# Performance work log

Measured on AMD Instinct MI355X. Metric: run time of the kernel, lower is better.

The kernel has to match this reference:

```python
import jax, jax.numpy as jnp
import numpy as np

HEAD, D_MODEL, D_KV = 16, 1024, 64
B, NQ, NK = 2, 2048, 2048


def setup_inputs() -> dict:
    key = jax.random.key(0)
    ks = jax.random.split(key, 10)
    s = 1.0 / np.sqrt(D_MODEL)
    return {
        "queries": jax.random.normal(ks[0], (B, NQ, D_MODEL), jnp.float32),
        "keys": jax.random.normal(ks[1], (B, NK, D_MODEL), jnp.float32),
        "values": jax.random.normal(ks[2], (B, NK, D_MODEL), jnp.float32),
        "group_prob": jax.random.uniform(ks[3], (B, 1, NQ, NK), jnp.float32),
        "attention_mask": jnp.ones((B, NK), jnp.int32),
        "Wq": jax.random.normal(ks[4], (D_MODEL, HEAD * D_KV), jnp.float32) * s,
        "bq": jnp.zeros((HEAD * D_KV,), jnp.float32),
        "Wk": jax.random.normal(ks[5], (D_MODEL, HEAD * D_KV), jnp.float32) * s,
        "bk": jnp.zeros((HEAD * D_KV,), jnp.float32),
        "Wv": jax.random.normal(ks[6], (D_MODEL, HEAD * D_KV), jnp.float32) * s,
        "bv": jnp.zeros((HEAD * D_KV,), jnp.float32),
    }


def reference(queries, keys, values, group_prob, attention_mask, Wq, bq, Wk, bk, Wv, bv):
    b_s, nq, _ = queries.shape
    nk = keys.shape[1]
    # projections -> [b, h, n, d]
    q = (queries @ Wq + bq).reshape(b_s, nq, HEAD, D_KV).transpose(0, 2, 1, 3)
    k = (keys @ Wk + bk).reshape(b_s, nk, HEAD, D_KV).transpose(0, 2, 1, 3)
    v = (values @ Wv + bv).reshape(b_s, nk, HEAD, D_KV).transpose(0, 2, 1, 3)
    att = jnp.einsum("bhqd,bhkd->bhqk", q, k) / np.sqrt(D_KV).astype(np.float32)
    # NOTE: original uses non-in-place `att.masked_fill(...)` and discards the
    # result, so attention_mask has NO effect on the computation. Replicated.
    att = jax.nn.softmax(att, axis=-1)
    att = att * group_prob  # post-softmax group gating, broadcast over heads
    out = jnp.einsum("bhqk,bhkd->bhqd", att, v)
    return out.transpose(0, 2, 1, 3).reshape(b_s, nq, D_MODEL)
```

## Files before the change

kernel.cpp:

```cpp
#include <hip/hip_runtime.h>
#include <hip/hip_bf16.h>
#include <cstdint>

typedef unsigned short ushort_t;
typedef __attribute__((ext_vector_type(8))) short short8;
typedef __attribute__((ext_vector_type(4))) float floatx4;
typedef __attribute__((ext_vector_type(4))) unsigned short ushort4_t;

#define H_   16
#define DKV_ 64
#define DM_  1024
#define B_   2
#define NQ_  2048
#define NK_  2048

__device__ __forceinline__ unsigned short f2bf(float f) {
  union { float f; unsigned int u; } v; v.f = f;
  unsigned int u = v.u;
  return (unsigned short)((u + 0x7fffu + ((u >> 16) & 1u)) >> 16);
}

__device__ __forceinline__ float fexp2(float x) { return __builtin_amdgcn_exp2f(x); }
__device__ __forceinline__ float frcp(float x)  { return __builtin_amdgcn_rcpf(x); }

__device__ __forceinline__ floatx4 mfma16(short8 a, short8 b, floatx4 c) {
  return __builtin_amdgcn_mfma_f32_16x16x32_bf16(a, b, c, 0, 0, 0);
}

__device__ __forceinline__ void gload_lds16(const ushort_t* g, ushort_t* l) {
  __builtin_amdgcn_global_load_lds(
      (const __attribute__((address_space(1))) void*)g,
      (__attribute__((address_space(3))) void*)l, 16, 0, 0);
}

__global__ __launch_bounds__(256) void cast_x_kernel(
    const float* __restrict__ q, const float* __restrict__ k,
    const float* __restrict__ v, ushort_t* __restrict__ dst)
{
  const int t = blockIdx.y;
  const float* src = (t == 0) ? q : (t == 1) ? k : v;
  ushort_t* d = dst + (size_t)t * 4096 * 1024;
  const int gid = blockIdx.x * 256 + threadIdx.x;
  #pragma unroll
  for (int u = 0; u < 8; u++) {
    const int i4 = u * 131072 + gid;
    floatx4 f = ((const floatx4*)src)[i4];
    ushort4_t o;
    #pragma unroll
    for (int e = 0; e < 4; e++) o[e] = f2bf(f[e]);
    *(ushort4_t*)&d[(size_t)i4 * 4] = o;
  }
}

__global__ __launch_bounds__(256) void cast_wt_kernel(
    const float* __restrict__ Wq, const float* __restrict__ Wk,
    const float* __restrict__ Wv, ushort_t* __restrict__ WtAll)
{
  __shared__ ushort_t tile[32][33];
  const int t = blockIdx.z;
  const float* W = (t == 0) ? Wq : (t == 1) ? Wk : Wv;
  ushort_t* Wt = WtAll + (size_t)t * 1024 * 1024;
  const int n0 = blockIdx.x * 32, k0 = blockIdx.y * 32;
  const int tid = threadIdx.x, r = tid >> 3, c4 = (tid & 7) * 4;
  floatx4 f = *(const floatx4*)&W[(size_t)(k0 + r) * 1024 + n0 + c4];
  #pragma unroll
  for (int e = 0; e < 4; e++) tile[r][c4 + e] = f2bf(f[e]);
  __syncthreads();
  ushort4_t o;
  #pragma unroll
  for (int e = 0; e < 4; e++) o[e] = tile[c4 + e][r];
  *(ushort4_t*)&Wt[(size_t)(n0 + r) * 1024 + k0 + c4] = o;
}

__global__ __launch_bounds__(256, 2) void proj_kernel2(
    const ushort_t* __restrict__ Xbf, const ushort_t* __restrict__ WtAll,
    const float* __restrict__ bq, const float* __restrict__ bk,
    const float* __restrict__ bv,
    ushort_t* __restrict__ Qb, ushort_t* __restrict__ Kb, ushort_t* __restrict__ Vt)
{
  const int mode = blockIdx.z;
  const ushort_t* X  = Xbf  + (size_t)mode * 4096 * 1024;
  const ushort_t* Wt = WtAll + (size_t)mode * 1024 * 1024;
  const float* bias  = (mode == 0) ? bq : (mode == 1) ? bk : bv;
  ushort_t* dst      = (mode == 0) ? Qb : (mode == 1) ? Kb : Vt;

  __shared__ ushort_t SM[8192];
  ushort_t* SA = SM;
  ushort_t* SB = SM + 4096;

  const int tid = threadIdx.x, lane = tid & 63, wid = tid >> 6;
  const int c = lane & 15, g = lane >> 4;
  const int m0 = blockIdx.y * 128, n0 = blockIdx.x * 128;
  const int wm = wid & 1, wn = wid >> 1, mb = wm * 64, nb = wn * 64;
  const int srow = lane >> 2;
  const int schunk = (lane & 3) * 8;

  floatx4 acc[4][4];
  #pragma unroll
  for (int i = 0; i < 4; i++)
    #pragma unroll
    for (int j = 0; j < 4; j++) acc[i][j] = floatx4{0.f, 0.f, 0.f, 0.f};

  for (int k0 = 0; k0 < DM_; k0 += 32) {
    __syncthreads();
    #pragma unroll
    for (int u = 0; u < 2; u++) {
      const int t = wid * 2 + u;
      gload_lds16(&X [(size_t)(m0 + t * 16 + srow) * 1024 + k0 + schunk], &SA[t * 512]);
      gload_lds16(&Wt[(size_t)(n0 + t * 16 + srow) * 1024 + k0 + schunk], &SB[t * 512]);
    }
    __syncthreads();

    short8 af[4], bfr[4];
    #pragma unroll
    for (int i = 0; i < 4; i++) af[i]  = *(const short8*)&SA[(mb + i * 16 + c) * 32 + g * 8];
    #pragma unroll
    for (int j = 0; j < 4; j++) bfr[j] = *(const short8*)&SB[(nb + j * 16 + c) * 32 + g * 8];
    #pragma unroll
    for (int i = 0; i < 4; i++)
      #pragma unroll
      for (int j = 0; j < 4; j++) acc[i][j] = mfma16(af[i], bfr[j], acc[i][j]);
  }

  __syncthreads();
  const float scale = (mode == 0) ? 0.18033688011112042f : 1.0f;
  ushort_t* EP = SM + wid * 2048;
  const int hh = (n0 + nb) >> 6;

  if (mode != 2) {
    for (int jj = 0; jj < 2; jj++) {
      #pragma unroll
      for (int jt = 0; jt < 2; jt++) {
        const int j = jj * 2 + jt;
        const float bb = bias[n0 + nb + j * 16 + c];
        #pragma unroll
        for (int i = 0; i < 4; i++)
          #pragma unroll
          for (int r = 0; r < 4; r++)
            EP[(i * 16 + g * 4 + r) * 32 + jt * 16 + c] =
                f2bf((acc[i][j][r] + bb) * scale);
      }
      #pragma unroll
      for (int u = 0; u < 8; u++) {
        const int rowl = u * 8 + (lane >> 3);
        ushort4_t vv = *(ushort4_t*)&EP[rowl * 32 + (lane & 7) * 4];
        const int rowg = m0 + mb + rowl;
        const int bb2 = rowg >> 11, nn = rowg & 2047;
        *(ushort4_t*)&dst[((size_t)(bb2 * H_ + hh) * NQ_ + nn) * DKV_ +
                          jj * 32 + (lane & 7) * 4] = vv;
      }
    }
  } else {
    const int bb2 = (m0 + mb) >> 11, nloc = (m0 + mb) & 2047;
    for (int j = 0; j < 4; j++) {
      const float bb = bias[n0 + nb + j * 16 + c];
      #pragma unroll
      for (int i = 0; i < 4; i++) {
        ushort4_t pk;
        #pragma unroll
        for (int r = 0; r < 4; r++) pk[r] = f2bf(acc[i][j][r] + bb);
        *(ushort4_t*)&EP[c * 72 + i * 16 + g * 4] = pk;
      }
      const int d0 = j * 16;
      #pragma unroll
      for (int u = 0; u < 2; u++) {
        const int coll = u * 8 + (lane >> 3);
        short8 vv = *(const short8*)&EP[coll * 72 + (lane & 7) * 8];
        *(short8*)&dst[((size_t)(bb2 * H_ + hh) * DKV_ + d0 + coll) * NK_ +
                       nloc + (lane & 7) * 8] = vv;
      }
    }
  }
}

constexpr int LDT = 40;
__global__ __launch_bounds__(256, 2) void proj_kernel_fb(
    const float* __restrict__ Xq, const float* __restrict__ Xk, const float* __restrict__ Xv,
    const float* __restrict__ Wq, const float* __restrict__ Wk, const float* __restrict__ Wv,
    const float* __restrict__ bq, const float* __restrict__ bk, const float* __restrict__ bv,
    ushort_t* __restrict__ Qb, ushort_t* __restrict__ Kb, ushort_t* __restrict__ Vt)
{
  const int mode = blockIdx.z;
  const float* X    = (mode == 0) ? Xq : (mode == 1) ? Xk : Xv;
  const float* W    = (mode == 0) ? Wq : (mode == 1) ? Wk : Wv;
  const float* bias = (mode == 0) ? bq : (mode == 1) ? bk : bv;
  ushort_t* dst     = (mode == 0) ? Qb : (mode == 1) ? Kb : Vt;

  __shared__ ushort_t Asm[128 * LDT];
  __shared__ ushort_t Bsm[128 * LDT];

  const int tid = threadIdx.x, lane = tid & 63, wid = tid >> 6;
  const int m0 = blockIdx.y * 128, n0 = blockIdx.x * 128;
  const int c = lane & 15, g = lane >> 4;
  const int wm = wid & 1, wn = wid >> 1, mb = wm * 64, nb = wn * 64;

  floatx4 acc[4][4];
  #pragma unroll
  for (int i = 0; i < 4; i++)
    #pragma unroll
    for (int j = 0; j < 4; j++) acc[i][j] = floatx4{0.f, 0.f, 0.f, 0.f};

  const int ar = tid >> 1, ah = tid & 1;
  const int bn = tid & 127, bh2 = tid >> 7;

  for (int k0 = 0; k0 < DM_; k0 += 32) {
    const floatx4* ap = (const floatx4*)(X + (size_t)(m0 + ar) * DM_ + k0 + ah * 16);
    floatx4 av0 = ap[0], av1 = ap[1], av2 = ap[2], av3 = ap[3];
    const float* wp = W + (size_t)(k0 + bh2 * 16) * 1024 + n0 + bn;
    float wv[16];
    #pragma unroll
    for (int j = 0; j < 16; j++) wv[j] = wp[j * 1024];
    short8 pa0, pa1, pb0, pb1;
    #pragma unroll
    for (int j = 0; j < 4; j++) {
      pa0[j] = (short)f2bf(av0[j]); pa0[4 + j] = (short)f2bf(av1[j]);
      pa1[j] = (short)f2bf(av2[j]); pa1[4 + j] = (short)f2bf(av3[j]);
    }
    #pragma unroll
    for (int j = 0; j < 8; j++) { pb0[j] = (short)f2bf(wv[j]); pb1[j] = (short)f2bf(wv[8 + j]); }
    __syncthreads();
    *(short8*)&Asm[ar * LDT + ah * 16]      = pa0;
    *(short8*)&Asm[ar * LDT + ah * 16 + 8]  = pa1;
    *(short8*)&Bsm[bn * LDT + bh2 * 16]     = pb0;
    *(short8*)&Bsm[bn * LDT + bh2 * 16 + 8] = pb1;
    __syncthreads();
    short8 af[4], bfr[4];
    #pragma unroll
    for (int i = 0; i < 4; i++) af[i]  = *(const short8*)&Asm[(mb + i * 16 + c) * LDT + g * 8];
    #pragma unroll
    for (int j = 0; j < 4; j++) bfr[j] = *(const short8*)&Bsm[(nb + j * 16 + c) * LDT + g * 8];
    #pragma unroll
    for (int i = 0; i < 4; i++)
      #pragma unroll
      for (int j = 0; j < 4; j++) acc[i][j] = mfma16(af[i], bfr[j], acc[i][j]);
  }
  #pragma unroll
  for (int j = 0; j < 4; j++) {
    const int col = n0 + nb + j * 16 + c;
    const float bv_ = bias[col];
    const int h = col >> 6, d = col & 63;
    #pragma unroll
    for (int i = 0; i < 4; i++)
      #pragma unroll
      for (int r = 0; r < 4; r++) {
        const int row = m0 + mb + i * 16 + g * 4 + r;
        const int b = row >> 11, n = row & 2047;
        float v = acc[i][j][r] + bv_;
        if (mode == 0) {
          v *= 0.18033688011112042f;
          dst[((size_t)(b * H_ + h) * NQ_ + n) * DKV_ + d] = f2bf(v);
        } else if (mode == 1) {
          dst[((size_t)(b * H_ + h) * NQ_ + n) * DKV_ + d] = f2bf(v);
        } else {
          dst[((size_t)(b * H_ + h) * DKV_ + d) * NK_ + n] = f2bf(v);
        }
      }
  }
}

__global__ __launch_bounds__(256, 2) void attn_kernel(
    const ushort_t* __restrict__ Qb, const ushort_t* __restrict__ Kb,
    const ushort_t* __restrict__ Vt, const float* __restrict__ gp,
    float* __restrict__ out)
{
  __shared__ ushort_t Ks[2][64 * 72];
  __shared__ ushort_t Vs[2][64 * 72];
  __shared__ ushort_t Pl[4][32 * 72];

  const int tid = threadIdx.x, lane = tid & 63, wid = tid >> 6;
  const int c = lane & 15, g = lane >> 4;
  const int h = blockIdx.x, b = blockIdx.z;
  const int bh = b * H_ + h;
  const int qw = blockIdx.y * 128 + wid * 32;

  const ushort_t* Qp = Qb + (size_t)bh * NQ_ * DKV_;
  const ushort_t* Kp = Kb + (size_t)bh * NK_ * DKV_;
  const ushort_t* Vp = Vt + (size_t)bh * DKV_ * NK_;
  const float* gpp = gp + (size_t)b * NQ_ * NK_ + (size_t)qw * NK_;
  ushort_t* Pw = Pl[wid];

  const int srow = wid * 16 + (lane >> 2);
  const int scol = (lane & 3) * 8;

  short8 qf[2][2];
  #pragma unroll
  for (int i = 0; i < 2; i++)
    #pragma unroll
    for (int kc = 0; kc < 2; kc++)
      qf[i][kc] = *(const short8*)&Qp[(qw + i * 16 + c) * DKV_ + kc * 32 + g * 8];

  #pragma unroll
  for (int half = 0; half < 2; half++) {
    short8 kv = *(const short8*)&Kp[(size_t)srow * DKV_ + scol + half * 32];
    short8 vv = *(const short8*)&Vp[(size_t)srow * NK_ + scol + half * 32];
    *(short8*)&Ks[0][srow * 72 + scol + half * 32] = kv;
    *(short8*)&Vs[0][srow * 72 + scol + half * 32] = vv;
  }
  __syncthreads();

  floatx4 o[2][4];
  float l[2][4];
  #pragma unroll
  for (int i = 0; i < 2; i++) {
    #pragma unroll
    for (int jd = 0; jd < 4; jd++) o[i][jd] = floatx4{0.f, 0.f, 0.f, 0.f};
    #pragma unroll
    for (int r = 0; r < 4; r++) l[i][r] = 0.f;
  }

  for (int t = 0; t < NK_ / 64; t++) {
    const int k0 = t * 64;
    const int cur = t & 1, nxt = cur ^ 1;

    float gpv[2][4][4];
    #pragma unroll
    for (int i = 0; i < 2; i++)
      #pragma unroll
      for (int r = 0; r < 4; r++) {
        const float* gq = gpp + (size_t)(i * 16 + g * 4 + r) * NK_ + k0 + c;
        #pragma unroll
        for (int jk = 0; jk < 4; jk++) gpv[i][jk][r] = gq[jk * 16];
      }

    short8 knx[2], vnx[2];
    const bool has_next = (t + 1) < NK_ / 64;
    if (has_next) {
      const int k1 = k0 + 64;
      #pragma unroll
      for (int half = 0; half < 2; half++) {
        knx[half] = *(const short8*)&Kp[(size_t)(k1 + srow) * DKV_ + scol + half * 32];
        vnx[half] = *(const short8*)&Vp[(size_t)srow * NK_ + k1 + scol + half * 32];
      }
    }

    floatx4 s[2][4];
    #pragma unroll
    for (int i = 0; i < 2; i++)
      #pragma unroll
      for (int jk = 0; jk < 4; jk++) s[i][jk] = floatx4{0.f, 0.f, 0.f, 0.f};
    #pragma unroll
    for (int jk = 0; jk < 4; jk++) {
      #pragma unroll
      for (int kc = 0; kc < 2; kc++) {
        short8 kf = *(const short8*)&Ks[cur][(jk * 16 + c) * 72 + kc * 32 + g * 8];
        #pragma unroll
        for (int i = 0; i < 2; i++) s[i][jk] = mfma16(qf[i][kc], kf, s[i][jk]);
      }
    }

    #pragma unroll
    for (int i = 0; i < 2; i++)
      #pragma unroll
      for (int jk = 0; jk < 4; jk++)
        #pragma unroll
        for (int r = 0; r < 4; r++) {
          const float p = fexp2(s[i][jk][r]);
          l[i][r] += p;
          Pw[(i * 16 + g * 4 + r) * 72 + jk * 16 + c] = f2bf(p * gpv[i][jk][r]);
        }

    #pragma unroll
    for (int kc = 0; kc < 2; kc++) {
      short8 af0 = *(const short8*)&Pw[(0 * 16 + c) * 72 + kc * 32 + g * 8];
      short8 af1 = *(const short8*)&Pw[(1 * 16 + c) * 72 + kc * 32 + g * 8];
      #pragma unroll
      for (int jd = 0; jd < 4; jd++) {
        short8 vf = *(const short8*)&Vs[cur][(jd * 16 + c) * 72 + kc * 32 + g * 8];
        o[0][jd] = mfma16(af0, vf, o[0][jd]);
        o[1][jd] = mfma16(af1, vf, o[1][jd]);
      }
    }

    if (has_next) {
      #pragma unroll
      for (int half = 0; half < 2; half++) {
        *(short8*)&Ks[nxt][srow * 72 + scol + half * 32] = knx[half];
        *(short8*)&Vs[nxt][srow * 72 + scol + half * 32] = vnx[half];
      }
    }
    __syncthreads();
  }

  float invl[2][4];
  #pragma unroll
  for (int i = 0; i < 2; i++)
    #pragma unroll
    for (int r = 0; r < 4; r++) {
      float rs = l[i][r];
      rs += __shfl_xor(rs, 1);
      rs += __shfl_xor(rs, 2);
      rs += __shfl_xor(rs, 4);
      rs += __shfl_xor(rs, 8);
      invl[i][r] = frcp(rs);
    }
  #pragma unroll
  for (int i = 0; i < 2; i++)
    #pragma unroll
    for (int jd = 0; jd < 4; jd++)
      #pragma unroll
      for (int r = 0; r < 4; r++) {
        const int row = qw + i * 16 + g * 4 + r;
        out[(size_t)(b * NQ_ + row) * 1024 + h * 64 + jd * 16 + c] =
            o[i][jd][r] * invl[i][r];
      }
}

extern "C" void kernel_launch(void* const* d_in, const int* in_sizes, int n_in,
                              void* d_out, int out_size, void* d_ws, size_t ws_size,
                              hipStream_t stream) {
  const float* queries = (const float*)d_in[0];
  const float* keys    = (const float*)d_in[1];
  const float* values  = (const float*)d_in[2];
  const float* gp      = (const float*)d_in[3];
  const float* Wq = (const float*)d_in[5];
  const float* bq = (const float*)d_in[6];
  const float* Wk = (const float*)d_in[7];
  const float* bk = (const float*)d_in[8];
  const float* Wv = (const float*)d_in[9];
  const float* bv = (const float*)d_in[10];

  const size_t SZ_QKV = (size_t)3 * B_ * H_ * NQ_ * DKV_;
  const size_t SZ_X   = (size_t)3 * 4096 * 1024;
  const size_t SZ_W   = (size_t)3 * 1024 * 1024;
  const size_t NEED   = (SZ_QKV + SZ_X + SZ_W) * sizeof(ushort_t);

  ushort_t* Qb = (ushort_t*)d_ws;
  ushort_t* Kb = Qb + (size_t)B_ * H_ * NQ_ * DKV_;
  ushort_t* Vt = Kb + (size_t)B_ * H_ * NK_ * DKV_;
  float* out = (float*)d_out;

  if (ws_size >= NEED) {
    ushort_t* Xbf = Qb + SZ_QKV;
    ushort_t* Wt  = Xbf + SZ_X;
    cast_x_kernel<<<dim3(512, 3), 256, 0, stream>>>(queries, keys, values, Xbf);
    cast_wt_kernel<<<dim3(32, 32, 3), 256, 0, stream>>>(Wq, Wk, Wv, Wt);
    proj_kernel2<<<dim3(8, 32, 3), 256, 0, stream>>>(
        Xbf, Wt, bq, bk, bv, Qb, Kb, Vt);
  } else {
    proj_kernel_fb<<<dim3(8, 32, 3), 256, 0, stream>>>(
        queries, keys, values, Wq, Wk, Wv, bq, bk, bv, Qb, Kb, Vt);
  }
  attn_kernel<<<dim3(H_, NQ_ / 128, B_), 256, 0, stream>>>(Qb, Kb, Vt, gp, out);
}
```

Baseline: 252.9 us.

## Split attention block into 8 waves of 16 query rows with swizzled P tile

The attention kernel now runs 512 threads per block, with each of 8 waves owning 16 query rows instead of 4 waves owning 32. K/V tile staging is spread across all 512 threads, one short8 per thread. The per-wave P scratch is smaller and uses an XOR column swizzle on write and read to cut LDS bank conflicts. This lowers registers per wave and raises the number of waves available to hide latency, but each K/V fragment read from LDS now feeds half as many MFMAs, so LDS traffic per FLOP goes up.

```diff
diff --git a/kernel.cpp b/kernel.cpp
--- a/kernel.cpp
+++ b/kernel.cpp
@@ -258,20 +258,20 @@
   }
 }
 
-__global__ __launch_bounds__(256, 2) void attn_kernel(
+__global__ __launch_bounds__(512, 4) void attn_kernel(
     const ushort_t* __restrict__ Qb, const ushort_t* __restrict__ Kb,
     const ushort_t* __restrict__ Vt, const float* __restrict__ gp,
     float* __restrict__ out)
 {
   __shared__ ushort_t Ks[2][64 * 72];
   __shared__ ushort_t Vs[2][64 * 72];
-  __shared__ ushort_t Pl[4][32 * 72];
+  __shared__ ushort_t Pl[8][16 * 72];
 
   const int tid = threadIdx.x, lane = tid & 63, wid = tid >> 6;
   const int c = lane & 15, g = lane >> 4;
   const int h = blockIdx.x, b = blockIdx.z;
   const int bh = b * H_ + h;
-  const int qw = blockIdx.y * 128 + wid * 32;
+  const int qw = blockIdx.y * 128 + wid * 16;
 
   const ushort_t* Qp = Qb + (size_t)bh * NQ_ * DKV_;
   const ushort_t* Kp = Kb + (size_t)bh * NK_ * DKV_;
@@ -279,130 +279,105 @@
   const float* gpp = gp + (size_t)b * NQ_ * NK_ + (size_t)qw * NK_;
   ushort_t* Pw = Pl[wid];
 
-  const int srow = wid * 16 + (lane >> 2);
-  const int scol = (lane & 3) * 8;
-
-  short8 qf[2][2];
-  #pragma unroll
-  for (int i = 0; i < 2; i++)
-    #pragma unroll
-    for (int kc = 0; kc < 2; kc++)
-      qf[i][kc] = *(const short8*)&Qp[(qw + i * 16 + c) * DKV_ + kc * 32 + g * 8];
-
-  #pragma unroll
-  for (int half = 0; half < 2; half++) {
-    short8 kv = *(const short8*)&Kp[(size_t)srow * DKV_ + scol + half * 32];
-    short8 vv = *(const short8*)&Vp[(size_t)srow * NK_ + scol + half * 32];
-    *(short8*)&Ks[0][srow * 72 + scol + half * 32] = kv;
-    *(short8*)&Vs[0][srow * 72 + scol + half * 32] = vv;
-  }
+  const int gx16 = (g >> 1) << 4;
+  const int prd  = g ^ (((c >> 3) & 1) << 1);
+
+  const int srow = tid >> 3;
+  const int scol = (tid & 7) * 8;
+
+  short8 qf[2];
+  #pragma unroll
+  for (int kc = 0; kc < 2; kc++)
+    qf[kc] = *(const short8*)&Qp[(qw + c) * DKV_ + kc * 32 + g * 8];
+
+  *(short8*)&Ks[0][srow * 72 + scol] = *(const short8*)&Kp[(size_t)srow * DKV_ + scol];
+  *(short8*)&Vs[0][srow * 72 + scol] = *(const short8*)&Vp[(size_t)srow * NK_ + scol];
   __syncthreads();
 
-  floatx4 o[2][4];
-  float l[2][4];
-  #pragma unroll
-  for (int i = 0; i < 2; i++) {
-    #pragma unroll
-    for (int jd = 0; jd < 4; jd++) o[i][jd] = floatx4{0.f, 0.f, 0.f, 0.f};
-    #pragma unroll
-    for (int r = 0; r < 4; r++) l[i][r] = 0.f;
-  }
+  floatx4 o[4];
+  float l[4];
+  #pragma unroll
+  for (int jd = 0; jd < 4; jd++) o[jd] = floatx4{0.f, 0.f, 0.f, 0.f};
+  #pragma unroll
+  for (int r = 0; r < 4; r++) l[r] = 0.f;
 
   for (int t = 0; t < NK_ / 64; t++) {
     const int k0 = t * 64;
     const int cur = t & 1, nxt = cur ^ 1;
 
-    float gpv[2][4][4];
-    #pragma unroll
-    for (int i = 0; i < 2; i++)
-      #pragma unroll
-      for (int r = 0; r < 4; r++) {
-        const float* gq = gpp + (size_t)(i * 16 + g * 4 + r) * NK_ + k0 + c;
-        #pragma unroll
-        for (int jk = 0; jk < 4; jk++) gpv[i][jk][r] = gq[jk * 16];
-      }
-
-    short8 knx[2], vnx[2];
+    float gpv[4][4];
+    #pragma unroll
+    for (int r = 0; r < 4; r++) {
+      const float* gq = gpp + (size_t)(g * 4 + r) * NK_ + k0 + c;
+      #pragma unroll
+      for (int jk = 0; jk < 4; jk++) gpv[jk][r] = gq[jk * 16];
+    }
+
+    short8 knx, vnx;
     const bool has_next = (t + 1) < NK_ / 64;
     if (has_next) {
       const int k1 = k0 + 64;
-      #pragma unroll
-      for (int half = 0; half < 2; half++) {
-        knx[half] = *(const short8*)&Kp[(size_t)(k1 + srow) * DKV_ + scol + half * 32];
-        vnx[half] = *(const short8*)&Vp[(size_t)srow * NK_ + k1 + scol + half * 32];
-      }
-    }
-
-    floatx4 s[2][4];
-    #pragma unroll
-    for (int i = 0; i < 2; i++)
-      #pragma unroll
-      for (int jk = 0; jk < 4; jk++) s[i][jk] = floatx4{0.f, 0.f, 0.f, 0.f};
-    #pragma unroll
-    for (int jk = 0; jk < 4; jk++) {
+      knx = *(const short8*)&Kp[(size_t)(k1 + srow) * DKV_ + scol];
+      vnx = *(const short8*)&Vp[(size_t)srow * NK_ + k1 + scol];
+    }
+
+    floatx4 s[4];
+    #pragma unroll
+    for (int jk = 0; jk < 4; jk++) s[jk] = floatx4{0.f, 0.f, 0.f, 0.f};
+    #pragma unroll
+    for (int jk = 0; jk < 4; jk++)
       #pragma unroll
       for (int kc = 0; kc < 2; kc++) {
         short8 kf = *(const short8*)&Ks[cur][(jk * 16 + c) * 72 + kc * 32 + g * 8];
-        #pragma unroll
-        for (int i = 0; i < 2; i++) s[i][jk] = mfma16(qf[i][kc], kf, s[i][jk]);
-      }
-    }
-
-    #pragma unroll
-    for (int i = 0; i < 2; i++)
-      #pragma unroll
-      for (int jk = 0; jk < 4; jk++)
-        #pragma unroll
-        for (int r = 0; r < 4; r++) {
-          const float p = fexp2(s[i][jk][r]);
-          l[i][r] += p;
-          Pw[(i * 16 + g * 4 + r) * 72 + jk * 16 + c] = f2bf(p * gpv[i][jk][r]);
-        }
+        s[jk] = mfma16(qf[kc], kf, s[jk]);
+      }
+
+    #pragma unroll
+    for (int jk = 0; jk < 4; jk++) {
+      const int colw = (jk << 4) ^ gx16;
+      #pragma unroll
+      for (int r = 0; r < 4; r++) {
+        const float p = fexp2(s[jk][r]);
+        l[r] += p;
+        Pw[(g * 4 + r) * 72 + colw + c] = f2bf(p * gpv[jk][r]);
+      }
+    }
 
     #pragma unroll
     for (int kc = 0; kc < 2; kc++) {
-      short8 af0 = *(const short8*)&Pw[(0 * 16 + c) * 72 + kc * 32 + g * 8];
-      short8 af1 = *(const short8*)&Pw[(1 * 16 + c) * 72 + kc * 32 + g * 8];
+      short8 af = *(const short8*)&Pw[c * 72 + kc * 32 + prd * 8];
       #pragma unroll
       for (int jd = 0; jd < 4; jd++) {
         short8 vf = *(const short8*)&Vs[cur][(jd * 16 + c) * 72 + kc * 32 + g * 8];
-        o[0][jd] = mfma16(af0, vf, o[0][jd]);
-        o[1][jd] = mfma16(af1, vf, o[1][jd]);
+        o[jd] = mfma16(af, vf, o[jd]);
       }
     }
 
     if (has_next) {
-      #pragma unroll
-      for (int half = 0; half < 2; half++) {
-        *(short8*)&Ks[nxt][srow * 72 + scol + half * 32] = knx[half];
-        *(short8*)&Vs[nxt][srow * 72 + scol + half * 32] = vnx[half];
-      }
+      *(short8*)&Ks[nxt][srow * 72 + scol] = knx;
+      *(short8*)&Vs[nxt][srow * 72 + scol] = vnx;
     }
     __syncthreads();
   }
 
-  float invl[2][4];
-  #pragma unroll
-  for (int i = 0; i < 2; i++)
+  float invl[4];
+  #pragma unroll
+  for (int r = 0; r < 4; r++) {
+    float rs = l[r];
+    rs += __shfl_xor(rs, 1);
+    rs += __shfl_xor(rs, 2);
+    rs += __shfl_xor(rs, 4);
+    rs += __shfl_xor(rs, 8);
+    invl[r] = frcp(rs);
+  }
+  #pragma unroll
+  for (int jd = 0; jd < 4; jd++)
     #pragma unroll
     for (int r = 0; r < 4; r++) {
-      float rs = l[i][r];
-      rs += __shfl_xor(rs, 1);
-      rs += __shfl_xor(rs, 2);
-      rs += __shfl_xor(rs, 4);
-      rs += __shfl_xor(rs, 8);
-      invl[i][r] = frcp(rs);
-    }
-  #pragma unroll
-  for (int i = 0; i < 2; i++)
-    #pragma unroll
-    for (int jd = 0; jd < 4; jd++)
-      #pragma unroll
-      for (int r = 0; r < 4; r++) {
-        const int row = qw + i * 16 + g * 4 + r;
-        out[(size_t)(b * NQ_ + row) * 1024 + h * 64 + jd * 16 + c] =
-            o[i][jd][r] * invl[i][r];
-      }
+      const int row = qw + g * 4 + r;
+      out[(size_t)(b * NQ_ + row) * 1024 + h * 64 + jd * 16 + c] =
+          o[jd][r] * invl[r];
+    }
 }
 
 extern "C" void kernel_launch(void* const* d_in, const int* in_sizes, int n_in,
@@ -440,5 +415,5 @@
     proj_kernel_fb<<<dim3(8, 32, 3), 256, 0, stream>>>(
         queries, keys, values, Wq, Wk, Wv, bq, bk, bv, Qb, Kb, Vt);
   }
-  attn_kernel<<<dim3(H_, NQ_ / 128, B_), 256, 0, stream>>>(Qb, Kb, Vt, gp, out);
-}
+  attn_kernel<<<dim3(H_, NQ_ / 128, B_), 512, 0, stream>>>(Qb, Kb, Vt, gp, out);
+}
```

Measured after the change: 245.6 us. -2.9%, faster.
